# Performance work log

Measured on AMD Instinct MI355X. Metric: run time of the kernel, lower is better.

## Reference

```python
import jax, jax.numpy as jnp
import numpy as np

NEG_INF = -1e9  # large negative for masking (avoid NaN rows under -inf with fully masked rows)
LEAKY_SLOPE = 0.2

def setup_inputs() -> dict:
    key = jax.random.key(0)
    k1, k2, k3, k4, k5 = jax.random.split(key, 5)
    N, in_dim, out_dim = 8192, 512, 64
    x = jax.random.normal(k1, (N, in_dim), dtype=jnp.float32)
    adj = jax.random.randint(k2, (N, N), 0, 2, dtype=jnp.int32)
    W = jax.random.normal(k3, (out_dim, in_dim), dtype=jnp.float32) * (1.0 / np.sqrt(in_dim))
    a_src = jax.random.normal(k4, (out_dim,), dtype=jnp.float32)
    a_dst = jax.random.normal(k5, (out_dim,), dtype=jnp.float32)
    return {"x": x, "adj": adj, "W": W, "a_src": a_src, "a_dst": a_dst}

def reference(x, adj, W, a_src, a_dst):
    # Linear projection: Wh[n, d]
    Wh = x @ W.T
    # Additive GAT attention: e[i, j] = LeakyReLU(a_src . Wh_i + a_dst . Wh_j)
    s = Wh @ a_src  # [N]
    d = Wh @ a_dst  # [N]
    e = jax.nn.leaky_relu(s[:, None] + d[None, :], negative_slope=LEAKY_SLOPE)  # [N, N]
    e = jnp.where(adj > 0, e, NEG_INF)
    alpha = jax.nn.softmax(e, axis=1)  # [N, N]
    # Dropout on alpha is identity in eval/reference mode.
    h_prime = alpha @ Wh  # [N, out_dim]
    return h_prime
```

## Files before the change

kernel.cpp:

```cpp
#include <hip/hip_runtime.h>

#define GN 8192
#define IN_DIM 512
#define ODIM 64
#define SLOPE 0.2f
#define JSPLIT 16
#define JCH (GN / JSPLIT)
#define LSTRIDE 68
#define NTILE 4

typedef __attribute__((ext_vector_type(4))) float  f32x4;
typedef __attribute__((ext_vector_type(4))) int    i32x4;
typedef __attribute__((ext_vector_type(8))) short  bf16x8;
typedef __attribute__((ext_vector_type(4))) unsigned short u16x4;

static __device__ __forceinline__ float bf2f(unsigned short u) {
    return __uint_as_float(((unsigned)u) << 16);
}
static __device__ __forceinline__ unsigned short f2bf(float f) {
    union { float f; unsigned u; } c; c.f = f;
    unsigned b = c.u;
    return (unsigned short)((b + 0x7fffu + ((b >> 16) & 1u)) >> 16);
}

static __device__ __forceinline__ bf16x8 load8(const void* p, size_t off, int f32) {
    if (f32) {
        f32x4 lo = *(const f32x4*)((const float*)p + off);
        f32x4 hi = *(const f32x4*)((const float*)p + off + 4);
        bf16x8 r;
        #pragma unroll
        for (int q = 0; q < 4; ++q) {
            r[q]     = (short)f2bf(lo[q]);
            r[4 + q] = (short)f2bf(hi[q]);
        }
        return r;
    }
    return *(const bf16x8*)((const ushort*)p + off);
}

extern "C" __global__ __launch_bounds__(256)
void gat_proj(const void* __restrict__ x_, const void* __restrict__ W_,
              const void* __restrict__ as_, const void* __restrict__ ad_,
              ushort* __restrict__ WhT, float* __restrict__ s_arr,
              float* __restrict__ d_arr, int* __restrict__ dmax_bits,
              int* __restrict__ dflag)
{
    const int wave = threadIdx.x >> 6;
    const int lane = threadIdx.x & 63;
    unsigned xw = ((const unsigned*)x_)[lane];
    unsigned ef = (xw >> 23) & 0xffu;
    unsigned long long vt = __ballot(ef > 60u && ef < 180u);
    const int f32 = (__popcll(vt) >= 32) ? 1 : 0;
    if (blockIdx.x == 0 && threadIdx.x == 0) *dflag = f32;

    const int quad = lane >> 4;
    const int lq   = lane & 15;
    const int i0   = blockIdx.x * 64 + wave * 16;

    f32x4 acc[4] = {{0,0,0,0},{0,0,0,0},{0,0,0,0},{0,0,0,0}};
    const size_t arow = (size_t)(i0 + lq) * IN_DIM;
    #pragma unroll 2
    for (int k0 = 0; k0 < IN_DIM; k0 += 32) {
        const int kk = k0 + quad * 8;
        bf16x8 a  = load8(x_, arow + kk, f32);
        bf16x8 b0 = load8(W_, (size_t)( 0 + lq) * IN_DIM + kk, f32);
        bf16x8 b1 = load8(W_, (size_t)(16 + lq) * IN_DIM + kk, f32);
        bf16x8 b2 = load8(W_, (size_t)(32 + lq) * IN_DIM + kk, f32);
        bf16x8 b3 = load8(W_, (size_t)(48 + lq) * IN_DIM + kk, f32);
        acc[0] = __builtin_amdgcn_mfma_f32_16x16x32_bf16(a, b0, acc[0], 0, 0, 0);
        acc[1] = __builtin_amdgcn_mfma_f32_16x16x32_bf16(a, b1, acc[1], 0, 0, 0);
        acc[2] = __builtin_amdgcn_mfma_f32_16x16x32_bf16(a, b2, acc[2], 0, 0, 0);
        acc[3] = __builtin_amdgcn_mfma_f32_16x16x32_bf16(a, b3, acc[3], 0, 0, 0);
    }
    float av_s[4], av_d[4];
    #pragma unroll
    for (int t = 0; t < 4; ++t) {
        const int n = t * 16 + lq;
        av_s[t] = f32 ? ((const float*)as_)[n] : bf2f(((const ushort*)as_)[n]);
        av_d[t] = f32 ? ((const float*)ad_)[n] : bf2f(((const ushort*)ad_)[n]);
    }
    #pragma unroll
    for (int t = 0; t < 4; ++t) {
        u16x4 pk;
        #pragma unroll
        for (int r = 0; r < 4; ++r) pk[r] = f2bf(acc[t][r]);
        *(u16x4*)(WhT + (size_t)(t * 16 + lq) * GN + i0 + quad * 4) = pk;
    }
    float ps[4], pd[4];
    #pragma unroll
    for (int r = 0; r < 4; ++r) {
        float s = 0.f, d = 0.f;
        #pragma unroll
        for (int t = 0; t < 4; ++t) {
            s = fmaf(acc[t][r], av_s[t], s);
            d = fmaf(acc[t][r], av_d[t], d);
        }
        #pragma unroll
        for (int off = 1; off < 16; off <<= 1) {
            s += __shfl_xor(s, off);
            d += __shfl_xor(d, off);
        }
        ps[r] = s; pd[r] = d;
    }
    if (lq == 0) {
        float dmx = -1e30f;
        #pragma unroll
        for (int r = 0; r < 4; ++r) {
            s_arr[i0 + quad * 4 + r] = ps[r];
            d_arr[i0 + quad * 4 + r] = pd[r];
            dmx = fmaxf(dmx, pd[r]);
        }
        if (dmx > 0.f) atomicMax(dmax_bits, __float_as_int(dmx));
    }
}

extern "C" __global__ __launch_bounds__(256)
void gat_attn(const int* __restrict__ adj, const ushort* __restrict__ WhT,
              const float* __restrict__ s_arr, const float* __restrict__ d_arr,
              const int* __restrict__ dmax_bits,
              float* __restrict__ accum, float* __restrict__ lsum)
{
    __shared__ unsigned char mb[2][64 * LSTRIDE];
    const int b    = blockIdx.x;
    const int ib   = b & 127;
    const int js0  = b >> 7;
    const int wave = threadIdx.x >> 6;
    const int lane = threadIdx.x & 63;
    const int quad = lane >> 4;
    const int lq   = lane & 15;
    const int i0   = ib * 64;
    const int li   = wave * 16 + lq;
    const int i    = i0 + li;
    const float dmax = __int_as_float(*dmax_bits);
    const float si = s_arr[i];
    const float tbv = si + dmax;
    const float mi = fmaxf(tbv, SLOPE * tbv);

    const size_t adjbase = (size_t)i0 * GN + lane * 8;

    i32x4 ra[3], rb[3];
    auto pack = [&](const i32x4& va, const i32x4& vb, int c, int bufsel) {
        unsigned byte = 0;
        #pragma unroll
        for (int q = 0; q < 4; ++q) {
            byte |= (va[q] > 0 ? 1u : 0u) << q;
            byte |= (vb[q] > 0 ? 1u : 0u) << (4 + q);
        }
        mb[bufsel][(c * 4 + wave) * LSTRIDE + lane] = (unsigned char)byte;
    };

    f32x4 acc0 = {0,0,0,0}, acc1 = {0,0,0,0}, acc2 = {0,0,0,0}, acc3 = {0,0,0,0};
    f32x4 acc4 = {0,0,0,0};
    bf16x8 ones;
    #pragma unroll
    for (int q = 0; q < 8; ++q) ones[q] = (short)0x3F80;

    {
        const int jb = js0 * JCH;
        #pragma unroll
        for (int c = 0; c < 16; ++c) {
            const int* rp = adj + adjbase + (size_t)(c * 4 + wave) * GN + jb;
            ra[c % 3] = ((const i32x4*)rp)[0];
            rb[c % 3] = ((const i32x4*)rp)[1];
            if (c >= 2) pack(ra[(c - 2) % 3], rb[(c - 2) % 3], c - 2, 0);
        }
        pack(ra[14 % 3], rb[14 % 3], 14, 0);
        pack(ra[15 % 3], rb[15 % 3], 15, 0);
    }
    __syncthreads();

    int jpre = js0 * JCH + quad * 8;
    f32x4 dv0 = *(const f32x4*)(d_arr + jpre);
    f32x4 dv1 = *(const f32x4*)(d_arr + jpre + 4);
    bf16x8 b0 = *(const bf16x8*)(WhT + (size_t)( 0 + lq) * GN + jpre);
    bf16x8 b1 = *(const bf16x8*)(WhT + (size_t)(16 + lq) * GN + jpre);
    bf16x8 b2 = *(const bf16x8*)(WhT + (size_t)(32 + lq) * GN + jpre);
    bf16x8 b3 = *(const bf16x8*)(WhT + (size_t)(48 + lq) * GN + jpre);

    #pragma unroll 1
    for (int t = 0; t < NTILE; ++t) {
        const int jb   = (js0 + 4 * t) * JCH;
        const int jbn  = jb + 4 * JCH;
        const bool more = (t < NTILE - 1);
        const int buf  = t & 1, nbuf = buf ^ 1;

        #pragma unroll
        for (int it = 0; it < 16; ++it) {
            const int jn = (it < 15) ? (jb + (it + 1) * 32 + quad * 8)
                                     : (more ? (jbn + quad * 8) : (jb + quad * 8));
            f32x4 ndv0 = *(const f32x4*)(d_arr + jn);
            f32x4 ndv1 = *(const f32x4*)(d_arr + jn + 4);
            bf16x8 nb0 = *(const bf16x8*)(WhT + (size_t)( 0 + lq) * GN + jn);
            bf16x8 nb1 = *(const bf16x8*)(WhT + (size_t)(16 + lq) * GN + jn);
            bf16x8 nb2 = *(const bf16x8*)(WhT + (size_t)(32 + lq) * GN + jn);
            bf16x8 nb3 = *(const bf16x8*)(WhT + (size_t)(48 + lq) * GN + jn);
            if (more) {
                const int* rp = adj + adjbase + (size_t)(it * 4 + wave) * GN + jbn;
                ra[it % 3] = ((const i32x4*)rp)[0];
                rb[it % 3] = ((const i32x4*)rp)[1];
            }
            if (more && it >= 2)
                pack(ra[(it - 2) % 3], rb[(it - 2) % 3], it - 2, nbuf);
            unsigned bw = *(const unsigned*)(&mb[buf][li * LSTRIDE + it * 4]);
            const unsigned m8 = (bw >> (quad * 8)) & 0xffu;
            float w[8];
            #pragma unroll
            for (int q = 0; q < 4; ++q) {
                float e0 = si + dv0[q];
                e0 = fmaxf(e0, SLOPE * e0);
                float v0 = __expf(e0 - mi);
                w[q] = ((m8 >> q) & 1u) ? v0 : 0.f;
                float e1 = si + dv1[q];
                e1 = fmaxf(e1, SLOPE * e1);
                float v1 = __expf(e1 - mi);
                w[4 + q] = ((m8 >> (4 + q)) & 1u) ? v1 : 0.f;
            }
            bf16x8 af;
            #pragma unroll
            for (int q = 0; q < 8; ++q) af[q] = (short)f2bf(w[q]);
            acc0 = __builtin_amdgcn_mfma_f32_16x16x32_bf16(af, b0, acc0, 0, 0, 0);
            acc1 = __builtin_amdgcn_mfma_f32_16x16x32_bf16(af, b1, acc1, 0, 0, 0);
            acc2 = __builtin_amdgcn_mfma_f32_16x16x32_bf16(af, b2, acc2, 0, 0, 0);
            acc3 = __builtin_amdgcn_mfma_f32_16x16x32_bf16(af, b3, acc3, 0, 0, 0);
            acc4 = __builtin_amdgcn_mfma_f32_16x16x32_bf16(af, ones, acc4, 0, 0, 0);
            dv0 = ndv0; dv1 = ndv1; b0 = nb0; b1 = nb1; b2 = nb2; b3 = nb3;
        }
        if (more) {
            pack(ra[14 % 3], rb[14 % 3], 14, nbuf);
            pack(ra[15 % 3], rb[15 % 3], 15, nbuf);
        }
        __syncthreads();
    }

    const int orow = i0 + wave * 16 + quad * 4;
    if (lq == 0) {
        #pragma unroll
        for (int r = 0; r < 4; ++r) atomicAdd(&lsum[orow + r], acc4[r]);
    }
    #pragma unroll
    for (int r = 0; r < 4; ++r) {
        atomicAdd(&accum[(size_t)(orow + r) * ODIM +  0 + lq], acc0[r]);
        atomicAdd(&accum[(size_t)(orow + r) * ODIM + 16 + lq], acc1[r]);
        atomicAdd(&accum[(size_t)(orow + r) * ODIM + 32 + lq], acc2[r]);
        atomicAdd(&accum[(size_t)(orow + r) * ODIM + 48 + lq], acc3[r]);
    }
}

extern "C" __global__ __launch_bounds__(256)
void gat_final(const float* __restrict__ accum, const float* __restrict__ lsum,
               const int* __restrict__ flag, void* __restrict__ out)
{
    const int idx = blockIdx.x * 256 + threadIdx.x;
    const float v = accum[idx] / lsum[idx >> 6];
    if (*flag) ((float*)out)[idx] = v;
    else       ((ushort*)out)[idx] = f2bf(v);
}

extern "C" void kernel_launch(void* const* d_in, const int* in_sizes, int n_in,
                              void* d_out, int out_size, void* d_ws, size_t ws_size,
                              hipStream_t stream)
{
    const void* x     = d_in[0];
    const int*  adj   = (const int*)d_in[1];
    const void* W     = d_in[2];
    const void* a_src = d_in[3];
    const void* a_dst = d_in[4];

    char* ws = (char*)d_ws;
    size_t off = 0;
    float* accum = (float*)(ws + off);  off += (size_t)GN * ODIM * 4;
    float* lsum  = (float*)(ws + off);  off += (size_t)GN * 4;
    int* dmax_bits = (int*)(ws + off);  off += 128;
    size_t zero_bytes = off;
    int* dflag = (int*)(ws + off);      off += 128;
    float* s_arr = (float*)(ws + off);  off += (size_t)GN * 4;
    float* d_arr = (float*)(ws + off);  off += (size_t)GN * 4;
    ushort* WhT  = (ushort*)(ws + off); off += (size_t)ODIM * GN * 2;

    hipMemsetAsync(ws, 0, zero_bytes, stream);
    gat_proj<<<GN / 64, 256, 0, stream>>>(x, W, a_src, a_dst,
                                          WhT, s_arr, d_arr, dmax_bits, dflag);
    gat_attn<<<512, 256, 0, stream>>>(adj, WhT, s_arr, d_arr,
                                      dmax_bits, accum, lsum);
    gat_final<<<GN * ODIM / 256, 256, 0, stream>>>(accum, lsum, dflag, d_out);
}
```

Baseline: 441.0 us.

## Pack WhT into 8-column blocks and double attention grid with fewer tiles

The projection now writes Wh in a blocked layout where each group of 8 nodes holds 64 features times 8 contiguous bf16 values. The B-operand loads in the attention loop then read one contiguous 1 KB block instead of 64 rows strided by GN. The attention grid goes from 512 to 1024 blocks with 2 tiles each, and launch bounds request 4 blocks per CU to raise occupancy. The trade-off is more partial-sum atomics into accum and lsum, plus possible register pressure from the occupancy hint.

After: 446.7 us. About the same (+1.3%).

```diff
diff --git a/kernel.cpp b/kernel.cpp
--- a/kernel.cpp
+++ b/kernel.cpp
@@ -7,7 +7,7 @@
 #define JSPLIT 16
 #define JCH (GN / JSPLIT)
 #define LSTRIDE 68
-#define NTILE 4
+#define NTILE 2
 
 typedef __attribute__((ext_vector_type(4))) float  f32x4;
 typedef __attribute__((ext_vector_type(4))) int    i32x4;
@@ -41,7 +41,7 @@
 extern "C" __global__ __launch_bounds__(256)
 void gat_proj(const void* __restrict__ x_, const void* __restrict__ W_,
               const void* __restrict__ as_, const void* __restrict__ ad_,
-              ushort* __restrict__ WhT, float* __restrict__ s_arr,
+              ushort* __restrict__ WhTp, float* __restrict__ s_arr,
               float* __restrict__ d_arr, int* __restrict__ dmax_bits,
               int* __restrict__ dflag)
 {
@@ -84,7 +84,9 @@
         u16x4 pk;
         #pragma unroll
         for (int r = 0; r < 4; ++r) pk[r] = f2bf(acc[t][r]);
-        *(u16x4*)(WhT + (size_t)(t * 16 + lq) * GN + i0 + quad * 4) = pk;
+        const size_t hw = ((size_t)((i0 >> 3) + (quad >> 1)) * 64 + t * 16 + lq) * 8
+                          + (quad & 1) * 4;
+        *(u16x4*)(WhTp + hw) = pk;
     }
     float ps[4], pd[4];
     #pragma unroll
@@ -114,8 +116,8 @@
     }
 }
 
-extern "C" __global__ __launch_bounds__(256)
-void gat_attn(const int* __restrict__ adj, const ushort* __restrict__ WhT,
+extern "C" __global__ __launch_bounds__(256, 4)
+void gat_attn(const int* __restrict__ adj, const ushort* __restrict__ WhTp,
               const float* __restrict__ s_arr, const float* __restrict__ d_arr,
               const int* __restrict__ dmax_bits,
               float* __restrict__ accum, float* __restrict__ lsum)
@@ -172,28 +174,31 @@
     int jpre = js0 * JCH + quad * 8;
     f32x4 dv0 = *(const f32x4*)(d_arr + jpre);
     f32x4 dv1 = *(const f32x4*)(d_arr + jpre + 4);
-    bf16x8 b0 = *(const bf16x8*)(WhT + (size_t)( 0 + lq) * GN + jpre);
-    bf16x8 b1 = *(const bf16x8*)(WhT + (size_t)(16 + lq) * GN + jpre);
-    bf16x8 b2 = *(const bf16x8*)(WhT + (size_t)(32 + lq) * GN + jpre);
-    bf16x8 b3 = *(const bf16x8*)(WhT + (size_t)(48 + lq) * GN + jpre);
+    const ushort* bb0 = WhTp + ((size_t)((js0 * JCH) >> 3) + quad) * 512;
+    bf16x8 b0 = *(const bf16x8*)(bb0 + ( 0 + lq) * 8);
+    bf16x8 b1 = *(const bf16x8*)(bb0 + (16 + lq) * 8);
+    bf16x8 b2 = *(const bf16x8*)(bb0 + (32 + lq) * 8);
+    bf16x8 b3 = *(const bf16x8*)(bb0 + (48 + lq) * 8);
 
     #pragma unroll 1
     for (int t = 0; t < NTILE; ++t) {
-        const int jb   = (js0 + 4 * t) * JCH;
-        const int jbn  = jb + 4 * JCH;
+        const int jb   = (js0 + 8 * t) * JCH;
+        const int jbn  = jb + 8 * JCH;
         const bool more = (t < NTILE - 1);
         const int buf  = t & 1, nbuf = buf ^ 1;
 
         #pragma unroll
         for (int it = 0; it < 16; ++it) {
-            const int jn = (it < 15) ? (jb + (it + 1) * 32 + quad * 8)
-                                     : (more ? (jbn + quad * 8) : (jb + quad * 8));
+            const int jtb = (it < 15) ? jb : (more ? jbn : jb);
+            const int itn = (it < 15) ? (it + 1) : 0;
+            const int jn  = jtb + itn * 32 + quad * 8;
             f32x4 ndv0 = *(const f32x4*)(d_arr + jn);
             f32x4 ndv1 = *(const f32x4*)(d_arr + jn + 4);
-            bf16x8 nb0 = *(const bf16x8*)(WhT + (size_t)( 0 + lq) * GN + jn);
-            bf16x8 nb1 = *(const bf16x8*)(WhT + (size_t)(16 + lq) * GN + jn);
-            bf16x8 nb2 = *(const bf16x8*)(WhT + (size_t)(32 + lq) * GN + jn);
-            bf16x8 nb3 = *(const bf16x8*)(WhT + (size_t)(48 + lq) * GN + jn);
+            const ushort* nb = WhTp + ((size_t)(jtb >> 3) + itn * 4 + quad) * 512;
+            bf16x8 nb0 = *(const bf16x8*)(nb + ( 0 + lq) * 8);
+            bf16x8 nb1 = *(const bf16x8*)(nb + (16 + lq) * 8);
+            bf16x8 nb2 = *(const bf16x8*)(nb + (32 + lq) * 8);
+            bf16x8 nb3 = *(const bf16x8*)(nb + (48 + lq) * 8);
             if (more) {
                 const int* rp = adj + adjbase + (size_t)(it * 4 + wave) * GN + jbn;
                 ra[it % 3] = ((const i32x4*)rp)[0];
@@ -275,12 +280,12 @@
     int* dflag = (int*)(ws + off);      off += 128;
     float* s_arr = (float*)(ws + off);  off += (size_t)GN * 4;
     float* d_arr = (float*)(ws + off);  off += (size_t)GN * 4;
-    ushort* WhT  = (ushort*)(ws + off); off += (size_t)ODIM * GN * 2;
+    ushort* WhTp = (ushort*)(ws + off); off += (size_t)ODIM * GN * 2;
 
     hipMemsetAsync(ws, 0, zero_bytes, stream);
     gat_proj<<<GN / 64, 256, 0, stream>>>(x, W, a_src, a_dst,
-                                          WhT, s_arr, d_arr, dmax_bits, dflag);
-    gat_attn<<<512, 256, 0, stream>>>(adj, WhT, s_arr, d_arr,
-                                      dmax_bits, accum, lsum);
+                                          WhTp, s_arr, d_arr, dmax_bits, dflag);
+    gat_attn<<<1024, 256, 0, stream>>>(adj, WhTp, s_arr, d_arr,
+                                       dmax_bits, accum, lsum);
     gat_final<<<GN * ODIM / 256, 256, 0, stream>>>(accum, lsum, dflag, d_out);
 }
```
